# Performance work log

Measured on AMD Instinct MI355X. Metric: run time of the kernel, lower is better.

Reference implementation:

```python
import jax, jax.numpy as jnp
import numpy as np

V = 512          # num vertices
F = 64           # pair-feature dim (gpnn_channels in)
C = 64           # gpnn_channels out
E = 8192         # num edges (avg degree 16)


def setup_inputs() -> dict:
    key = jax.random.key(0)
    k1, k2, k3, k4 = jax.random.split(key, 4)
    alpha = jax.random.normal(k1, (V * V, F), dtype=jnp.float32)          # pair features, row v*V+w
    edge_index = jax.random.randint(k2, (2, E), 0, V)                      # COO [src; dst]
    # GPNNEdgeConv.nn = MLP([F, C, C], act='relu')  (norm treated as identity / eval stats)
    w1 = jax.random.normal(k3, (F, C), dtype=jnp.float32) * (1.0 / np.sqrt(F))
    b1 = jnp.zeros((C,), dtype=jnp.float32)
    w2 = jax.random.normal(k4, (C, C), dtype=jnp.float32) * (1.0 / np.sqrt(C))
    b2 = jnp.zeros((C,), dtype=jnp.float32)
    eps = jnp.asarray(0.0, dtype=jnp.float32)                              # train_eps parameter
    return {"alpha": alpha, "edge_index": edge_index,
            "w1": w1, "b1": b1, "w2": w2, "b2": b2, "eps": eps}


def reference(alpha, edge_index, w1, b1, w2, b2, eps):
    # Dense 0/1 adjacency adj_t: adj[v, j] = 1 iff edge j -> v (dst-indexed, as spmm(adj_t, .)).
    adj = jnp.zeros((V, V), dtype=alpha.dtype).at[edge_index[1], edge_index[0]].set(1.0)
    a3 = alpha.reshape(V, V, F)  # a3[v, j] = alpha[v*V + j]
    # message_and_aggregate: out[v*V+w] = row v of spmm(adj_t, A_{v,w}),
    # where A_{v,w}[j] = alpha[v*V+j] + alpha[w*V+j]  (sum aggregation)
    #   = sum_j adj[v,j] * (a3[v,j] + a3[w,j]) = S[v] + T[v,w]
    S = jnp.einsum('vj,vjf->vf', adj, a3)    # [V, F]
    T = jnp.einsum('vj,wjf->vwf', adj, a3)   # [V, V, F]
    out = (S[:, None, :] + T).reshape(V * V, F)
    # GINConv residual: out + (1 + eps) * x_r, then MLP (Linear-ReLU-Linear)
    out = out + (1.0 + eps) * alpha
    h = jax.nn.relu(out @ w1 + b1)
    return h @ w2 + b2
```

## Files before the change

### kernel.cpp

```cpp
#include <hip/hip_runtime.h>
#include <hip/hip_bf16.h>

#define NV 512
#define NF 64

typedef __attribute__((ext_vector_type(8))) short bf16x8;
typedef __attribute__((ext_vector_type(4))) float f32x4;

union BF8 { bf16x8 v; unsigned u[4]; };

__device__ __forceinline__ unsigned short f2bf(float x) {
    unsigned u = __float_as_uint(x);
    unsigned r = (u + 0x7fffu + ((u >> 16) & 1u)) >> 16;
    return (unsigned short)r;
}

__device__ __forceinline__ unsigned awt_addr(int f, int jbyte) {
    return (unsigned)((f * 1024 + jbyte) ^ (((f ^ (f >> 3)) & 7) << 4));
}
__device__ __forceinline__ unsigned wt_addr(int m, int n, int kbyte) {
    return (unsigned)(m * 8192 + ((n * 128 + kbyte) ^ (((n ^ (n >> 3)) & 7) << 4)));
}
__device__ __forceinline__ int scr_slot(int row) {
    return ((row >> 2) ^ ((row & 3) << 1)) & 7;
}

__global__ void k_edges(const int* __restrict__ ei, int E, unsigned int* __restrict__ mask) {
    int e = blockIdx.x * 256 + threadIdx.x;
    if (e < E) {
        int s = ei[e];
        int d = ei[E + e];
        atomicOr(&mask[d * 16 + (s >> 5)], 1u << (s & 31));
    }
}

__global__ void k_S(const unsigned int* __restrict__ mask, const float* __restrict__ alpha,
                    float* __restrict__ S) {
    __shared__ float red[4][64];
    int v = blockIdx.x;
    int lane = threadIdx.x & 63;
    int g = threadIdx.x >> 6;
    float a0 = 0.f, a1 = 0.f;
    for (int wd = g * 4; wd < g * 4 + 4; ++wd) {
        unsigned bits = mask[v * 16 + wd];
        while (bits) {
            int b0 = __ffs(bits) - 1; bits &= bits - 1;
            float x0 = alpha[((size_t)v * NV + wd * 32 + b0) * NF + lane];
            if (bits) {
                int b1 = __ffs(bits) - 1; bits &= bits - 1;
                a1 += alpha[((size_t)v * NV + wd * 32 + b1) * NF + lane];
            }
            a0 += x0;
        }
    }
    red[g][lane] = a0 + a1;
    __syncthreads();
    if (g == 0)
        S[v * NF + lane] = red[0][lane] + red[1][lane] + red[2][lane] + red[3][lane];
}


__global__ __launch_bounds__(512, 4) void k_main(
    const float* __restrict__ alpha, const float* __restrict__ w1, const float* __restrict__ b1,
    const float* __restrict__ w2, const float* __restrict__ b2, const float* __restrict__ eps_p,
    const unsigned int* __restrict__ mask, const float* __restrict__ S,
    float* __restrict__ out)
{
    extern __shared__ char smem[];

    const int w    = blockIdx.x;
    const int t    = threadIdx.x;
    const int lane = t & 63;
    const int wid  = t >> 6;
    const int nlo  = lane & 15;
    const int g    = lane >> 4;
    const int mbase = wid * 64;
    const float* src = alpha + (size_t)w * (NV * NF);

    auto stage_half = [&](int i) {
        int task = i * 512 + t;
        int jb = task >> 4;
        int fq = task & 15;
        unsigned ua[4][4];
#pragma unroll
        for (int h = 0; h < 4; ++h) {
            f32x4 r0 = *(const f32x4*)(src + (size_t)(jb * 8 + 2 * h) * NF + fq * 4);
            f32x4 r1 = *(const f32x4*)(src + (size_t)(jb * 8 + 2 * h + 1) * NF + fq * 4);
#pragma unroll
            for (int c = 0; c < 4; ++c)
                ua[c][h] = (unsigned)f2bf(r0[c]) | ((unsigned)f2bf(r1[c]) << 16);
        }
#pragma unroll
        for (int c = 0; c < 4; ++c) {
            BF8 p;
            p.u[0] = ua[c][0]; p.u[1] = ua[c][1]; p.u[2] = ua[c][2]; p.u[3] = ua[c][3];
            *(bf16x8*)(smem + awt_addr(fq * 4 + c, jb * 16)) = p.v;
        }
    };

    f32x4 acc[4][4];

    stage_half(0);

#pragma unroll
    for (int mi = 0; mi < 4; ++mi)
#pragma unroll
        for (int nt = 0; nt < 4; ++nt)
#pragma unroll
            for (int r = 0; r < 4; ++r)
                acc[mi][nt][r] = S[(size_t)(mbase + mi * 16 + g * 4 + r) * NF + nt * 16 + nlo];

    __syncthreads();

    auto gemm_q = [&](int kq) {
        unsigned qw[4][4];
#pragma unroll
        for (int mi = 0; mi < 4; ++mi) {
            const uint4 q = *(const uint4*)(mask + (size_t)(mbase + mi * 16 + nlo) * 16 + kq * 4);
            qw[mi][0] = q.x; qw[mi][1] = q.y; qw[mi][2] = q.z; qw[mi][3] = q.w;
        }
#pragma unroll
        for (int kr = 0; kr < 4; ++kr) {
            const int kk = kq * 4 + kr;
            BF8 afr[4];
#pragma unroll
            for (int mi = 0; mi < 4; ++mi) {
                unsigned byteb = (qw[mi][kr] >> (g * 8)) & 0xFFu;
#pragma unroll
                for (int h = 0; h < 4; ++h) {
                    unsigned b0 = (byteb >> (2 * h)) & 1u;
                    unsigned b1 = (byteb >> (2 * h + 1)) & 1u;
                    afr[mi].u[h] = (b0 ? 0x3F80u : 0u) | (b1 ? 0x3F800000u : 0u);
                }
            }
#pragma unroll
            for (int nt = 0; nt < 4; ++nt) {
                bf16x8 bfr = *(const bf16x8*)(smem + awt_addr(nt * 16 + nlo, kk * 64 + g * 16));
#pragma unroll
                for (int mi = 0; mi < 4; ++mi)
                    acc[mi][nt] = __builtin_amdgcn_mfma_f32_16x16x32_bf16(afr[mi].v, bfr, acc[mi][nt], 0, 0, 0);
            }
        }
    };

    stage_half(1);
    gemm_q(0);
    gemm_q(1);
    __syncthreads();
    gemm_q(2);
    gemm_q(3);
    __syncthreads();

    if (t < 256) {
        int m  = t >> 7;
        int sub = t & 127;
        int jb = sub >> 4;
        int fq = sub & 15;
        const float* wsrc = m ? w2 : w1;
        unsigned ua[4][4];
#pragma unroll
        for (int h = 0; h < 4; ++h) {
            f32x4 r0 = *(const f32x4*)(wsrc + (size_t)(jb * 8 + 2 * h) * NF + fq * 4);
            f32x4 r1 = *(const f32x4*)(wsrc + (size_t)(jb * 8 + 2 * h + 1) * NF + fq * 4);
#pragma unroll
            for (int c = 0; c < 4; ++c)
                ua[c][h] = (unsigned)f2bf(r0[c]) | ((unsigned)f2bf(r1[c]) << 16);
        }
#pragma unroll
        for (int c = 0; c < 4; ++c) {
            BF8 p;
            p.u[0] = ua[c][0]; p.u[1] = ua[c][1]; p.u[2] = ua[c][2]; p.u[3] = ua[c][3];
            *(bf16x8*)(smem + wt_addr(m, fq * 4 + c, jb * 16)) = p.v;
        }
    }
    float b1v[4], b2v[4];
#pragma unroll
    for (int nt = 0; nt < 4; ++nt) {
        b1v[nt] = b1[nt * 16 + nlo];
        b2v[nt] = b2[nt * 16 + nlo];
    }
    const float ceps = 1.0f + eps_p[0];

    float rvv[4][4];
#pragma unroll
    for (int nt = 0; nt < 4; ++nt)
#pragma unroll
        for (int r = 0; r < 4; ++r)
            rvv[nt][r] = alpha[((size_t)(mbase + g * 4 + r) * NV + w) * NF + nt * 16 + nlo];

    __syncthreads();

    char* myscr = smem + 16384 + wid * 2048;
#pragma unroll
    for (int mi = 0; mi < 4; ++mi) {
        int v0 = mbase + mi * 16;

        float rvc[4][4];
#pragma unroll
        for (int nt = 0; nt < 4; ++nt)
#pragma unroll
            for (int r = 0; r < 4; ++r) rvc[nt][r] = rvv[nt][r];

        if (mi < 3) {
#pragma unroll
            for (int nt = 0; nt < 4; ++nt)
#pragma unroll
                for (int r = 0; r < 4; ++r)
                    rvv[nt][r] = alpha[((size_t)(v0 + 16 + g * 4 + r) * NV + w) * NF + nt * 16 + nlo];
        }

#pragma unroll
        for (int nt = 0; nt < 4; ++nt) {
            int f = nt * 16 + nlo;
#pragma unroll
            for (int r = 0; r < 4; ++r) {
                float pre = acc[mi][nt][r] + ceps * rvc[nt][r];
                int row = g * 4 + r;
                *(unsigned short*)(myscr + row * 128 + ((2 * f) ^ (scr_slot(row) << 4))) = f2bf(pre);
            }
        }

        bf16x8 a0 = *(const bf16x8*)(myscr + nlo * 128 + ((g * 16) ^ (scr_slot(nlo) << 4)));
        bf16x8 a1 = *(const bf16x8*)(myscr + nlo * 128 + ((g * 16 + 64) ^ (scr_slot(nlo) << 4)));
        f32x4 accm[4];
#pragma unroll
        for (int nt = 0; nt < 4; ++nt) {
            bf16x8 wf0 = *(const bf16x8*)(smem + wt_addr(0, nt * 16 + nlo, g * 16));
            bf16x8 wf1 = *(const bf16x8*)(smem + wt_addr(0, nt * 16 + nlo, 64 + g * 16));
            f32x4 z = {0.f, 0.f, 0.f, 0.f};
            z = __builtin_amdgcn_mfma_f32_16x16x32_bf16(a0, wf0, z, 0, 0, 0);
            z = __builtin_amdgcn_mfma_f32_16x16x32_bf16(a1, wf1, z, 0, 0, 0);
            accm[nt] = z;
        }

#pragma unroll
        for (int nt = 0; nt < 4; ++nt)
#pragma unroll
            for (int r = 0; r < 4; ++r) {
                float hv = accm[nt][r] + b1v[nt];
                hv = hv > 0.f ? hv : 0.f;
                int row = g * 4 + r;
                *(unsigned short*)(myscr + row * 128 + ((2 * (nt * 16 + nlo)) ^ (scr_slot(row) << 4))) = f2bf(hv);
            }

        bf16x8 h0 = *(const bf16x8*)(myscr + nlo * 128 + ((g * 16) ^ (scr_slot(nlo) << 4)));
        bf16x8 h1 = *(const bf16x8*)(myscr + nlo * 128 + ((g * 16 + 64) ^ (scr_slot(nlo) << 4)));
#pragma unroll
        for (int nt = 0; nt < 4; ++nt) {
            bf16x8 wf0 = *(const bf16x8*)(smem + wt_addr(1, nt * 16 + nlo, g * 16));
            bf16x8 wf1 = *(const bf16x8*)(smem + wt_addr(1, nt * 16 + nlo, 64 + g * 16));
            f32x4 z = {0.f, 0.f, 0.f, 0.f};
            z = __builtin_amdgcn_mfma_f32_16x16x32_bf16(h0, wf0, z, 0, 0, 0);
            z = __builtin_amdgcn_mfma_f32_16x16x32_bf16(h1, wf1, z, 0, 0, 0);
#pragma unroll
            for (int r = 0; r < 4; ++r) {
                int vv = v0 + g * 4 + r;
                out[((size_t)vv * NV + w) * NF + nt * 16 + nlo] = z[r] + b2v[nt];
            }
        }
    }
}

extern "C" void kernel_launch(void* const* d_in, const int* in_sizes, int n_in,
                              void* d_out, int out_size, void* d_ws, size_t ws_size,
                              hipStream_t stream) {
    const float* alpha = (const float*)d_in[0];
    const int*   ei    = (const int*)d_in[1];
    const float* w1    = (const float*)d_in[2];
    const float* b1    = (const float*)d_in[3];
    const float* w2    = (const float*)d_in[4];
    const float* b2    = (const float*)d_in[5];
    const float* eps   = (const float*)d_in[6];
    float* out = (float*)d_out;
    int E = in_sizes[1] / 2;

    unsigned int* mask = (unsigned int*)d_ws;
    float* S = (float*)d_ws + 8192;

    hipMemsetAsync(mask, 0, 8192 * sizeof(unsigned int), stream);
    k_edges<<<(E + 255) / 256, 256, 0, stream>>>(ei, E, mask);
    k_S    <<<NV, 256, 0, stream>>>(mask, alpha, S);

    const int smem_bytes = 65536;
    hipFuncSetAttribute(reinterpret_cast<const void*>(k_main),
                        hipFuncAttributeMaxDynamicSharedMemorySize, smem_bytes);
    k_main <<<NV, 512, smem_bytes, stream>>>(alpha, w1, b1, w2, b2, eps, mask, S, out);
}
```

Measured before the change: 65.50 us.

## Split fused kernel into aggregation kernel writing bf16 pre-activations and separate MLP kernel

The single fused kernel is split in two. k_pre computes the adjacency GMM plus the residual and writes bf16 pre-activations to a 32 MB workspace buffer. k_mlp then runs the two-layer MLP over 1024 blocks, with weights held in registers. The aim is to relieve register and LDS pressure and to raise MLP parallelism and occupancy, at the cost of an extra global round-trip of the intermediate and one more launch. The fused kernel is kept as a fallback when the workspace is too small, and the LDS scratch swizzle function is also changed.

```diff
diff --git a/kernel.cpp b/kernel.cpp
--- a/kernel.cpp
+++ b/kernel.cpp
@@ -21,8 +21,8 @@
 __device__ __forceinline__ unsigned wt_addr(int m, int n, int kbyte) {
     return (unsigned)(m * 8192 + ((n * 128 + kbyte) ^ (((n ^ (n >> 3)) & 7) << 4)));
 }
-__device__ __forceinline__ int scr_slot(int row) {
-    return ((row >> 2) ^ ((row & 3) << 1)) & 7;
+__device__ __forceinline__ int slot2(int row) {
+    return 2 * (((row >> 2) ^ row) & 3) + (row & 1);
 }
 
 __global__ void k_edges(const int* __restrict__ ei, int E, unsigned int* __restrict__ mask) {
@@ -59,12 +59,10 @@
         S[v * NF + lane] = red[0][lane] + red[1][lane] + red[2][lane] + red[3][lane];
 }
 
-
-__global__ __launch_bounds__(512, 4) void k_main(
-    const float* __restrict__ alpha, const float* __restrict__ w1, const float* __restrict__ b1,
-    const float* __restrict__ w2, const float* __restrict__ b2, const float* __restrict__ eps_p,
+__global__ __launch_bounds__(512, 4) void k_pre(
+    const float* __restrict__ alpha, const float* __restrict__ eps_p,
     const unsigned int* __restrict__ mask, const float* __restrict__ S,
-    float* __restrict__ out)
+    char* __restrict__ preb)
 {
     extern __shared__ char smem[];
 
@@ -99,9 +97,7 @@
     };
 
     f32x4 acc[4][4];
-
     stage_half(0);
-
 #pragma unroll
     for (int mi = 0; mi < 4; ++mi)
 #pragma unroll
@@ -149,6 +145,205 @@
     __syncthreads();
     gemm_q(2);
     gemm_q(3);
+    __syncthreads();
+
+    const float ceps = 1.0f + eps_p[0];
+    char* myscr = smem + wid * 2048;
+    char* dstw  = preb + (size_t)w * 65536;
+
+#pragma unroll
+    for (int mi = 0; mi < 4; ++mi) {
+        int v0 = mbase + mi * 16;
+        float rvv[4][4];
+#pragma unroll
+        for (int nt = 0; nt < 4; ++nt)
+#pragma unroll
+            for (int r = 0; r < 4; ++r)
+                rvv[nt][r] = alpha[((size_t)(v0 + g * 4 + r) * NV + w) * NF + nt * 16 + nlo];
+
+#pragma unroll
+        for (int nt = 0; nt < 4; ++nt)
+#pragma unroll
+            for (int r = 0; r < 4; ++r) {
+                float pre = acc[mi][nt][r] + ceps * rvv[nt][r];
+                int row = g * 4 + r;
+                *(unsigned short*)(myscr + row * 128 + ((2 * (nt * 16 + nlo)) ^ (slot2(row) << 4))) = f2bf(pre);
+            }
+
+#pragma unroll
+        for (int it = 0; it < 2; ++it) {
+            int lin = it * 64 + lane;
+            int row = lin >> 3, ch = lin & 7;
+            bf16x8 vv = *(const bf16x8*)(myscr + row * 128 + ((ch * 16) ^ (slot2(row) << 4)));
+            *(bf16x8*)(dstw + (size_t)(v0 + row) * 128 + ch * 16) = vv;
+        }
+    }
+}
+
+__global__ __launch_bounds__(256, 4) void k_mlp(
+    const char* __restrict__ preb, const float* __restrict__ w1, const float* __restrict__ b1,
+    const float* __restrict__ w2, const float* __restrict__ b2, float* __restrict__ out)
+{
+    __shared__ char scr[4][2048];
+    const int b    = blockIdx.x;
+    const int w    = b >> 1;
+    const int vh   = b & 1;
+    const int t    = threadIdx.x;
+    const int lane = t & 63;
+    const int wid  = t >> 6;
+    const int nlo  = lane & 15;
+    const int g    = lane >> 4;
+    const int kbase = g * 8;
+
+    bf16x8 w1f[2][4], w2f[2][4];
+#pragma unroll
+    for (int ks = 0; ks < 2; ++ks)
+#pragma unroll
+        for (int nt = 0; nt < 4; ++nt) {
+            bf16x8 a, bb;
+#pragma unroll
+            for (int e = 0; e < 8; ++e) {
+                int k = ks * 32 + kbase + e;
+                a[e]  = (short)f2bf(w1[k * NF + nt * 16 + nlo]);
+                bb[e] = (short)f2bf(w2[k * NF + nt * 16 + nlo]);
+            }
+            w1f[ks][nt] = a;
+            w2f[ks][nt] = bb;
+        }
+    float b1v[4], b2v[4];
+#pragma unroll
+    for (int nt = 0; nt < 4; ++nt) {
+        b1v[nt] = b1[nt * 16 + nlo];
+        b2v[nt] = b2[nt * 16 + nlo];
+    }
+
+    const char* srcw = preb + (size_t)w * 65536 + (size_t)vh * 32768;
+    char* myscr = scr[wid];
+
+#pragma unroll
+    for (int mi = 0; mi < 4; ++mi) {
+        int rl0 = wid * 64 + mi * 16;
+
+        bf16x8 a0 = *(const bf16x8*)(srcw + (size_t)(rl0 + nlo) * 128 + g * 16);
+        bf16x8 a1 = *(const bf16x8*)(srcw + (size_t)(rl0 + nlo) * 128 + 64 + g * 16);
+        f32x4 accm[4];
+#pragma unroll
+        for (int nt = 0; nt < 4; ++nt) {
+            f32x4 z = {0.f, 0.f, 0.f, 0.f};
+            z = __builtin_amdgcn_mfma_f32_16x16x32_bf16(a0, w1f[0][nt], z, 0, 0, 0);
+            z = __builtin_amdgcn_mfma_f32_16x16x32_bf16(a1, w1f[1][nt], z, 0, 0, 0);
+            accm[nt] = z;
+        }
+
+#pragma unroll
+        for (int nt = 0; nt < 4; ++nt)
+#pragma unroll
+            for (int r = 0; r < 4; ++r) {
+                float hv = accm[nt][r] + b1v[nt];
+                hv = hv > 0.f ? hv : 0.f;
+                int row = g * 4 + r;
+                *(unsigned short*)(myscr + row * 128 + ((2 * (nt * 16 + nlo)) ^ (slot2(row) << 4))) = f2bf(hv);
+            }
+
+        bf16x8 h0 = *(const bf16x8*)(myscr + nlo * 128 + ((g * 16) ^ (slot2(nlo) << 4)));
+        bf16x8 h1 = *(const bf16x8*)(myscr + nlo * 128 + ((g * 16 + 64) ^ (slot2(nlo) << 4)));
+#pragma unroll
+        for (int nt = 0; nt < 4; ++nt) {
+            f32x4 z = {0.f, 0.f, 0.f, 0.f};
+            z = __builtin_amdgcn_mfma_f32_16x16x32_bf16(h0, w2f[0][nt], z, 0, 0, 0);
+            z = __builtin_amdgcn_mfma_f32_16x16x32_bf16(h1, w2f[1][nt], z, 0, 0, 0);
+#pragma unroll
+            for (int r = 0; r < 4; ++r) {
+                int v = vh * 256 + rl0 + g * 4 + r;
+                out[((size_t)v * NV + w) * NF + nt * 16 + nlo] = z[r] + b2v[nt];
+            }
+        }
+    }
+}
+
+__global__ __launch_bounds__(512, 4) void k_main(
+    const float* __restrict__ alpha, const float* __restrict__ w1, const float* __restrict__ b1,
+    const float* __restrict__ w2, const float* __restrict__ b2, const float* __restrict__ eps_p,
+    const unsigned int* __restrict__ mask, const float* __restrict__ S,
+    float* __restrict__ out)
+{
+    extern __shared__ char smem[];
+    const int w    = blockIdx.x;
+    const int t    = threadIdx.x;
+    const int lane = t & 63;
+    const int wid  = t >> 6;
+    const int nlo  = lane & 15;
+    const int g    = lane >> 4;
+    const int mbase = wid * 64;
+    const float* src = alpha + (size_t)w * (NV * NF);
+
+    auto stage_half = [&](int i) {
+        int task = i * 512 + t;
+        int jb = task >> 4;
+        int fq = task & 15;
+        unsigned ua[4][4];
+#pragma unroll
+        for (int h = 0; h < 4; ++h) {
+            f32x4 r0 = *(const f32x4*)(src + (size_t)(jb * 8 + 2 * h) * NF + fq * 4);
+            f32x4 r1 = *(const f32x4*)(src + (size_t)(jb * 8 + 2 * h + 1) * NF + fq * 4);
+#pragma unroll
+            for (int c = 0; c < 4; ++c)
+                ua[c][h] = (unsigned)f2bf(r0[c]) | ((unsigned)f2bf(r1[c]) << 16);
+        }
+#pragma unroll
+        for (int c = 0; c < 4; ++c) {
+            BF8 p;
+            p.u[0] = ua[c][0]; p.u[1] = ua[c][1]; p.u[2] = ua[c][2]; p.u[3] = ua[c][3];
+            *(bf16x8*)(smem + awt_addr(fq * 4 + c, jb * 16)) = p.v;
+        }
+    };
+
+    f32x4 acc[4][4];
+    stage_half(0);
+#pragma unroll
+    for (int mi = 0; mi < 4; ++mi)
+#pragma unroll
+        for (int nt = 0; nt < 4; ++nt)
+#pragma unroll
+            for (int r = 0; r < 4; ++r)
+                acc[mi][nt][r] = S[(size_t)(mbase + mi * 16 + g * 4 + r) * NF + nt * 16 + nlo];
+    __syncthreads();
+
+    auto gemm_q = [&](int kq) {
+        unsigned qw[4][4];
+#pragma unroll
+        for (int mi = 0; mi < 4; ++mi) {
+            const uint4 q = *(const uint4*)(mask + (size_t)(mbase + mi * 16 + nlo) * 16 + kq * 4);
+            qw[mi][0] = q.x; qw[mi][1] = q.y; qw[mi][2] = q.z; qw[mi][3] = q.w;
+        }
+#pragma unroll
+        for (int kr = 0; kr < 4; ++kr) {
+            const int kk = kq * 4 + kr;
+            BF8 afr[4];
+#pragma unroll
+            for (int mi = 0; mi < 4; ++mi) {
+                unsigned byteb = (qw[mi][kr] >> (g * 8)) & 0xFFu;
+#pragma unroll
+                for (int h = 0; h < 4; ++h) {
+                    unsigned b0 = (byteb >> (2 * h)) & 1u;
+                    unsigned b1 = (byteb >> (2 * h + 1)) & 1u;
+                    afr[mi].u[h] = (b0 ? 0x3F80u : 0u) | (b1 ? 0x3F800000u : 0u);
+                }
+            }
+#pragma unroll
+            for (int nt = 0; nt < 4; ++nt) {
+                bf16x8 bfr = *(const bf16x8*)(smem + awt_addr(nt * 16 + nlo, kk * 64 + g * 16));
+#pragma unroll
+                for (int mi = 0; mi < 4; ++mi)
+                    acc[mi][nt] = __builtin_amdgcn_mfma_f32_16x16x32_bf16(afr[mi].v, bfr, acc[mi][nt], 0, 0, 0);
+            }
+        }
+    };
+
+    stage_half(1);
+    gemm_q(0); gemm_q(1);
+    __syncthreads();
+    gemm_q(2); gemm_q(3);
     __syncthreads();
 
     if (t < 256) {
@@ -180,48 +375,28 @@
         b2v[nt] = b2[nt * 16 + nlo];
     }
     const float ceps = 1.0f + eps_p[0];
-
-    float rvv[4][4];
-#pragma unroll
-    for (int nt = 0; nt < 4; ++nt)
-#pragma unroll
-        for (int r = 0; r < 4; ++r)
-            rvv[nt][r] = alpha[((size_t)(mbase + g * 4 + r) * NV + w) * NF + nt * 16 + nlo];
-
     __syncthreads();
 
     char* myscr = smem + 16384 + wid * 2048;
 #pragma unroll
     for (int mi = 0; mi < 4; ++mi) {
         int v0 = mbase + mi * 16;
-
-        float rvc[4][4];
-#pragma unroll
-        for (int nt = 0; nt < 4; ++nt)
-#pragma unroll
-            for (int r = 0; r < 4; ++r) rvc[nt][r] = rvv[nt][r];
-
-        if (mi < 3) {
-#pragma unroll
-            for (int nt = 0; nt < 4; ++nt)
-#pragma unroll
-                for (int r = 0; r < 4; ++r)
-                    rvv[nt][r] = alpha[((size_t)(v0 + 16 + g * 4 + r) * NV + w) * NF + nt * 16 + nlo];
-        }
-
-#pragma unroll
-        for (int nt = 0; nt < 4; ++nt) {
-            int f = nt * 16 + nlo;
-#pragma unroll
-            for (int r = 0; r < 4; ++r) {
-                float pre = acc[mi][nt][r] + ceps * rvc[nt][r];
+        float rvv[4][4];
+#pragma unroll
+        for (int nt = 0; nt < 4; ++nt)
+#pragma unroll
+            for (int r = 0; r < 4; ++r)
+                rvv[nt][r] = alpha[((size_t)(v0 + g * 4 + r) * NV + w) * NF + nt * 16 + nlo];
+#pragma unroll
+        for (int nt = 0; nt < 4; ++nt)
+#pragma unroll
+            for (int r = 0; r < 4; ++r) {
+                float pre = acc[mi][nt][r] + ceps * rvv[nt][r];
                 int row = g * 4 + r;
-                *(unsigned short*)(myscr + row * 128 + ((2 * f) ^ (scr_slot(row) << 4))) = f2bf(pre);
-            }
-        }
-
-        bf16x8 a0 = *(const bf16x8*)(myscr + nlo * 128 + ((g * 16) ^ (scr_slot(nlo) << 4)));
-        bf16x8 a1 = *(const bf16x8*)(myscr + nlo * 128 + ((g * 16 + 64) ^ (scr_slot(nlo) << 4)));
+                *(unsigned short*)(myscr + row * 128 + ((2 * (nt * 16 + nlo)) ^ (slot2(row) << 4))) = f2bf(pre);
+            }
+        bf16x8 a0 = *(const bf16x8*)(myscr + nlo * 128 + ((g * 16) ^ (slot2(nlo) << 4)));
+        bf16x8 a1 = *(const bf16x8*)(myscr + nlo * 128 + ((g * 16 + 64) ^ (slot2(nlo) << 4)));
         f32x4 accm[4];
 #pragma unroll
         for (int nt = 0; nt < 4; ++nt) {
@@ -232,7 +407,6 @@
             z = __builtin_amdgcn_mfma_f32_16x16x32_bf16(a1, wf1, z, 0, 0, 0);
             accm[nt] = z;
         }
-
 #pragma unroll
         for (int nt = 0; nt < 4; ++nt)
 #pragma unroll
@@ -240,11 +414,10 @@
                 float hv = accm[nt][r] + b1v[nt];
                 hv = hv > 0.f ? hv : 0.f;
                 int row = g * 4 + r;
-                *(unsigned short*)(myscr + row * 128 + ((2 * (nt * 16 + nlo)) ^ (scr_slot(row) << 4))) = f2bf(hv);
-            }
-
-        bf16x8 h0 = *(const bf16x8*)(myscr + nlo * 128 + ((g * 16) ^ (scr_slot(nlo) << 4)));
-        bf16x8 h1 = *(const bf16x8*)(myscr + nlo * 128 + ((g * 16 + 64) ^ (scr_slot(nlo) << 4)));
+                *(unsigned short*)(myscr + row * 128 + ((2 * (nt * 16 + nlo)) ^ (slot2(row) << 4))) = f2bf(hv);
+            }
+        bf16x8 h0 = *(const bf16x8*)(myscr + nlo * 128 + ((g * 16) ^ (slot2(nlo) << 4)));
+        bf16x8 h1 = *(const bf16x8*)(myscr + nlo * 128 + ((g * 16 + 64) ^ (slot2(nlo) << 4)));
 #pragma unroll
         for (int nt = 0; nt < 4; ++nt) {
             bf16x8 wf0 = *(const bf16x8*)(smem + wt_addr(1, nt * 16 + nlo, g * 16));
@@ -275,14 +448,22 @@
     int E = in_sizes[1] / 2;
 
     unsigned int* mask = (unsigned int*)d_ws;
-    float* S = (float*)d_ws + 8192;
-
-    hipMemsetAsync(mask, 0, 8192 * sizeof(unsigned int), stream);
+    float* S = (float*)((char*)d_ws + 32768);
+    char*  preb = (char*)d_ws + 163840;
+    const size_t need = 163840 + (size_t)NV * 65536;
+
+    hipMemsetAsync(mask, 0, 32768, stream);
     k_edges<<<(E + 255) / 256, 256, 0, stream>>>(ei, E, mask);
     k_S    <<<NV, 256, 0, stream>>>(mask, alpha, S);
 
-    const int smem_bytes = 65536;
-    hipFuncSetAttribute(reinterpret_cast<const void*>(k_main),
-                        hipFuncAttributeMaxDynamicSharedMemorySize, smem_bytes);
-    k_main <<<NV, 512, smem_bytes, stream>>>(alpha, w1, b1, w2, b2, eps, mask, S, out);
-}
+    if (ws_size >= need) {
+        hipFuncSetAttribute(reinterpret_cast<const void*>(k_pre),
+                            hipFuncAttributeMaxDynamicSharedMemorySize, 65536);
+        k_pre<<<NV, 512, 65536, stream>>>(alpha, eps, mask, S, preb);
+        k_mlp<<<NV * 2, 256, 0, stream>>>(preb, w1, b1, w2, b2, out);
+    } else {
+        hipFuncSetAttribute(reinterpret_cast<const void*>(k_main),
+                            hipFuncAttributeMaxDynamicSharedMemorySize, 65536);
+        k_main<<<NV, 512, 65536, stream>>>(alpha, w1, b1, w2, b2, eps, mask, S, out);
+    }
+}
```

After: 85.75 us. +30.9%, slower.
